# Performance work log

Hardware: AMD Instinct MI355X
Metric: run time of the kernel (lower is better)

## Reference

```python
import jax, jax.numpy as jnp
import numpy as np

D = 4544
H = 71
DKV = 64  # D // H
NKV = 1   # multi-query: one shared KV head
ROPE_BASE = 10000.0


def setup_inputs() -> dict:
    key = jax.random.key(0)
    k1, k2, k3 = jax.random.split(key, 3)
    N, L = 2, 1024
    hidden_states = jax.random.normal(k1, (N, L, D), dtype=jnp.float32)
    W_qkv = jax.random.normal(k2, (D + 2 * NKV * DKV, D), dtype=jnp.float32) * (D ** -0.5)
    W_dense = jax.random.normal(k3, (D, D), dtype=jnp.float32) * (D ** -0.5)
    return {"hidden_states": hidden_states, "W_qkv": W_qkv, "W_dense": W_dense}


def _rope_cos_sin(L, dtype):
    inv_freq = 1.0 / (ROPE_BASE ** (jnp.arange(0, DKV, 2, dtype=jnp.float32) / DKV))  # [Dkv/2]
    t = jnp.arange(L, dtype=jnp.float32)
    freqs = jnp.outer(t, inv_freq)                 # [L, Dkv/2]
    emb = jnp.concatenate((freqs, freqs), axis=1)  # [L, Dkv]
    cos = jnp.cos(emb)[None, None, :, :].astype(dtype)  # [1,1,L,Dkv]
    sin = jnp.sin(emb)[None, None, :, :].astype(dtype)
    return cos, sin


def _rotate_half(x):
    half = x.shape[-1] // 2
    return jnp.concatenate((-x[..., half:], x[..., :half]), axis=-1)


def reference(hidden_states, W_qkv, W_dense):
    N, L, _ = hidden_states.shape
    # Fused QKV projection (no bias): [N, L, D + 2*Dkv]
    fused = jnp.einsum('nld,ed->nle', hidden_states, W_qkv)
    fused = fused.reshape(N, L, H + 2 * NKV, DKV)
    query = jnp.transpose(fused[:, :, : H, :], (0, 2, 1, 3))            # [N, H, L, Dkv]
    key_h = jnp.transpose(fused[:, :, H : H + NKV, :], (0, 2, 1, 3))    # [N, 1, L, Dkv]
    value = jnp.transpose(fused[:, :, H + NKV :, :], (0, 2, 1, 3))      # [N, 1, L, Dkv]

    # RoPE (prefill path: positions 0..L-1)
    cos, sin = _rope_cos_sin(L, query.dtype)
    query = query * cos + _rotate_half(query) * sin
    key_h = key_h * cos + _rotate_half(key_h) * sin

    # Causal SDPA with multi-query KV broadcast (scale = 1/sqrt(Dkv))
    k = key_h[:, 0]    # [N, L, Dkv]
    v = value[:, 0]    # [N, L, Dkv]
    scale = 1.0 / jnp.sqrt(jnp.asarray(DKV, dtype=query.dtype))
    scores = jnp.einsum('nhqd,nkd->nhqk', query, k) * scale  # [N, H, L, L]
    causal = jnp.tril(jnp.ones((L, L), dtype=bool))
    scores = jnp.where(causal[None, None], scores, jnp.finfo(scores.dtype).min)
    weights = jax.nn.softmax(scores, axis=-1)
    attn = jnp.einsum('nhqk,nkd->nhqd', weights, v)           # [N, H, L, Dkv]

    attn = jnp.transpose(attn, (0, 2, 1, 3)).reshape(N, L, H * DKV)  # [N, L, D]
    out = jnp.einsum('nld,ed->nle', attn, W_dense)
    return out
```

## Files before the change

### kernel.cpp

```cpp
#include <hip/hip_runtime.h>

#define D_MODEL 4544
#define E_QKV   4672
#define E_STR   4736
#define E_PAD2  4864
#define D_PAD   4608
#define NH      71
#define SEQ     1024
#define NB      2
#define M_ROWS  2048

typedef __bf16 bf16_t;
typedef bf16_t bf16x8 __attribute__((ext_vector_type(8)));
typedef float f32x4 __attribute__((ext_vector_type(4)));
typedef float f32x16 __attribute__((ext_vector_type(16)));
typedef unsigned u32x4 __attribute__((ext_vector_type(4)));

typedef __attribute__((address_space(1))) const void* gas_ptr;
typedef __attribute__((address_space(3))) void* las_ptr;

static __device__ __forceinline__ unsigned short f2bf(float f) {
  union { float f; unsigned u; } v; v.f = f;
  unsigned r = (v.u + 0x7fffu + ((v.u >> 16) & 1u)) >> 16;
  return (unsigned short)r;
}

static __device__ __forceinline__ unsigned cvtpk_bf16(float lo, float hi) {
  unsigned r;
  asm("v_cvt_pk_bf16_f32 %0, %1, %2" : "=v"(r) : "v"(lo), "v"(hi));
  return r;
}

static __device__ __forceinline__ float fast_exp2(float x) {
  float r;
  asm("v_exp_f32 %0, %1" : "=v"(r) : "v"(x));
  return r;
}

__global__ void convert_pad(const float* __restrict__ src, unsigned short* __restrict__ dst,
                            int rows_src, int rows_pad, int cols) {
  int idx = blockIdx.x * 256 + threadIdx.x;
  int cols4 = cols >> 2;
  int total = rows_pad * cols4;
  if (idx >= total) return;
  int row = idx / cols4;
  int c4 = (idx - row * cols4) << 2;
  ushort4 o;
  if (row < rows_src) {
    const float4 v = *(const float4*)(src + (size_t)row * cols + c4);
    o.x = f2bf(v.x); o.y = f2bf(v.y); o.z = f2bf(v.z); o.w = f2bf(v.w);
  } else {
    o.x = 0; o.y = 0; o.z = 0; o.w = 0;
  }
  *(ushort4*)(dst + (size_t)row * cols + c4) = o;
}

#define REGION(b_, op_, kh_) (((((b_)*2+(op_))*2)+(kh_)) << 13)

#define STAGE(b_, op_, kh_, kt_) do {                                          \
  const unsigned short* _src = (op_) ? B : A;                                  \
  const size_t _rb = (op_) ? bCol : bRow;                                      \
  _Pragma("unroll")                                                            \
  for (int _ld = 0; _ld < 2; ++_ld) {                                          \
    int _ch = _ld * 512 + tid;                                                 \
    const unsigned short* _ga = _src + (_rb + (_ch >> 2)) * K                  \
                                + (kt_) * 64 + (kh_) * 32 + ((_ch & 3) << 3);  \
    __builtin_amdgcn_global_load_lds((gas_ptr)_ga,                             \
        (las_ptr)(lds + REGION(b_, op_, kh_) + ((_ld * 512 + wave * 64) << 3)),\
        16, 0, 0);                                                             \
  }                                                                            \
} while (0)

#define LDA4(b_, kh_, mh_) do {                                                \
  const unsigned short* _ab = lds + REGION(b_, 0, kh_);                        \
  _Pragma("unroll")                                                            \
  for (int _mm = 0; _mm < 4; ++_mm)                                            \
    a[_mm] = *(const bf16x8*)&_ab[(wm * 128 + (mh_) * 64 + _mm * 16 + c) * 32 + g * 8]; \
} while (0)

#define LDB4(b_, kh_) do {                                                     \
  const unsigned short* _bp = lds + REGION(b_, 1, kh_);                        \
  _Pragma("unroll")                                                            \
  for (int _n = 0; _n < 4; ++_n)                                               \
    bv[_n] = *(const bf16x8*)&_bp[(wn * 64 + _n * 16 + c) * 32 + g * 8];       \
} while (0)

#define MFMA16(mh_) do {                                                       \
  _Pragma("unroll")                                                            \
  for (int _mm = 0; _mm < 4; ++_mm)                                            \
    _Pragma("unroll")                                                          \
    for (int _n = 0; _n < 4; ++_n)                                             \
      acc[(mh_) * 4 + _mm][_n] = __builtin_amdgcn_mfma_f32_16x16x32_bf16(      \
          a[_mm], bv[_n], acc[(mh_) * 4 + _mm][_n], 0, 0, 0);                  \
} while (0)

__global__ __launch_bounds__(512, 2) void gemm256(
    const unsigned short* __restrict__ A,
    const unsigned short* __restrict__ B,
    float* __restrict__ C,
    int K, int Ntiles, int ldc, int Nact) {
  __shared__ __align__(16) unsigned short lds[65536];
  const int tid = threadIdx.x;
  const int wave = tid >> 6, lane = tid & 63;
  const int g = lane >> 4, c = lane & 15;
  const int wm = wave >> 2, wn = wave & 3;
  const int nwg = gridDim.x;
  const int swz = (blockIdx.x & 7) * (nwg >> 3) + (blockIdx.x >> 3);
  const int bm = swz / Ntiles, bn = swz - bm * Ntiles;
  const size_t bRow = (size_t)bm * 256, bCol = (size_t)bn * 256;
  const int NT = K >> 6;

  f32x4 acc[8][4] = {};

  STAGE(0, 0, 0, 0); STAGE(0, 1, 0, 0); STAGE(0, 0, 1, 0); STAGE(0, 1, 1, 0);
  STAGE(1, 1, 0, 1); STAGE(1, 0, 0, 1); STAGE(1, 1, 1, 1);
  asm volatile("s_waitcnt vmcnt(6)" ::: "memory");
  __builtin_amdgcn_s_barrier();

  for (int t = 0; t < NT; ++t) {
    const int b = t & 1;
    const int tn1 = (t + 1 < NT) ? t + 1 : 0;
    const int tn2 = (t + 2 < NT) ? t + 2 : 0;
    bf16x8 a[4], bv[4];
    LDA4(b, 0, 0); LDB4(b, 0);
    STAGE(b ^ 1, 0, 1, tn1);
    __builtin_amdgcn_s_barrier();
    asm volatile("s_waitcnt lgkmcnt(0)" ::: "memory");
    __builtin_amdgcn_s_setprio(1);
    MFMA16(0);
    __builtin_amdgcn_s_setprio(0);
    __builtin_amdgcn_s_barrier();
    LDA4(b, 0, 1);
    STAGE(b, 1, 0, tn2);
    __builtin_amdgcn_s_barrier();
    asm volatile("s_waitcnt lgkmcnt(0)" ::: "memory");
    __builtin_amdgcn_s_setprio(1);
    MFMA16(1);
    __builtin_amdgcn_s_setprio(0);
    __builtin_amdgcn_s_barrier();
    LDA4(b, 1, 0); LDB4(b, 1);
    STAGE(b, 0, 0, tn2);
    __builtin_amdgcn_s_barrier();
    asm volatile("s_waitcnt lgkmcnt(0)" ::: "memory");
    __builtin_amdgcn_s_setprio(1);
    MFMA16(0);
    __builtin_amdgcn_s_setprio(0);
    __builtin_amdgcn_s_barrier();
    LDA4(b, 1, 1);
    STAGE(b, 1, 1, tn2);
    __builtin_amdgcn_s_barrier();
    asm volatile("s_waitcnt lgkmcnt(0)" ::: "memory");
    __builtin_amdgcn_s_setprio(1);
    MFMA16(1);
    __builtin_amdgcn_s_setprio(0);
    asm volatile("s_waitcnt vmcnt(6)" ::: "memory");
    __builtin_amdgcn_s_barrier();
  }
  asm volatile("s_waitcnt vmcnt(0)" ::: "memory");

#pragma unroll
  for (int mm = 0; mm < 8; ++mm) {
#pragma unroll
    for (int n = 0; n < 4; ++n) {
      int col = (int)bCol + wn * 64 + n * 16 + c;
      if (col < Nact) {
#pragma unroll
        for (int r = 0; r < 4; ++r) {
          size_t row = bRow + wm * 128 + mm * 16 + g * 4 + r;
          C[row * ldc + col] = acc[mm][n][r];
        }
      }
    }
  }
}

__global__ void rope_extract(const float* __restrict__ fused,
                             unsigned short* __restrict__ Qb,
                             unsigned short* __restrict__ Kb,
                             unsigned short* __restrict__ VTb) {
  int idx = blockIdx.x * 256 + threadIdx.x;
  const int total = NB * SEQ * 73 * 64;
  if (idx >= total) return;
  int d = idx & 63;
  int t = idx >> 6;
  int h = t % 73;  t /= 73;
  int l = t & (SEQ - 1);
  int n = t >> 10;
  const float* frow = fused + ((size_t)(n * SEQ + l)) * E_STR + h * 64;
  float x = frow[d];
  if (h == 72) {
    VTb[((size_t)(n * 64 + d)) * SEQ + l] = f2bf(x);
    return;
  }
  int dh = d & 31;
  float inv = __expf(-(float)dh * (9.210340371976184f / 32.0f));
  float ang = (float)l * inv;
  float sn, cs;
  __sincosf(ang, &sn, &cs);
  float xr = frow[(d < 32) ? d + 32 : d - 32];
  float rh = (d < 32) ? -xr : xr;
  float out = x * cs + rh * sn;
  if (h == 71) {
    Kb[((size_t)(n * SEQ + l)) * 64 + d] = f2bf(out);
  } else {
    Qb[(((size_t)(n * NH + h)) * SEQ + l) * 64 + d] = f2bf(out * 0.1803368801111204f);
  }
}

__global__ __launch_bounds__(128) void attn_kernel(
    const unsigned short* __restrict__ Qb,
    const unsigned short* __restrict__ Kb,
    const unsigned short* __restrict__ VTb,
    unsigned short* __restrict__ attnb) {
  const int h = blockIdx.y, n = blockIdx.z;
  const int wave = threadIdx.x >> 6, lane = threadIdx.x & 63;
  const int c = lane & 31, hi = lane >> 5;
  const int gw = blockIdx.x * 2 + wave;

  const unsigned short* kbase = Kb + (size_t)n * SEQ * 64;
  const unsigned short* vtbase = VTb + (size_t)n * 64 * SEQ;

  for (int pass = 0; pass < 2; ++pass) {
    const int tile = pass ? gw : (31 - gw);
    const int qrow0 = tile * 32;
    const int q = qrow0 + c;
    const unsigned short* qbase = Qb + (((size_t)(n * NH + h)) * SEQ + qrow0) * 64;

    bf16x8 qf[4];
#pragma unroll
    for (int cc = 0; cc < 4; ++cc)
      qf[cc] = *(const bf16x8*)&qbase[c * 64 + cc * 16 + hi * 8];

    f32x16 o0 = {}, o1 = {};
    float m_run = -1e30f, l_run = 0.f;

    for (int kt = 0; kt < qrow0 + 32; kt += 64) {
      f32x16 s0 = {}, s1 = {};
#pragma unroll
      for (int cc = 0; cc < 4; ++cc) {
        bf16x8 k0 = *(const bf16x8*)&kbase[(size_t)(kt + c) * 64 + cc * 16 + hi * 8];
        bf16x8 k1 = *(const bf16x8*)&kbase[(size_t)(kt + 32 + c) * 64 + cc * 16 + hi * 8];
        s0 = __builtin_amdgcn_mfma_f32_32x32x16_bf16(k0, qf[cc], s0, 0, 0, 0);
        s1 = __builtin_amdgcn_mfma_f32_32x32x16_bf16(k1, qf[cc], s1, 0, 0, 0);
      }
      if (kt + 63 > qrow0) {
#pragma unroll
        for (int r = 0; r < 16; ++r) {
          const int key0 = kt + (r & 3) + 8 * (r >> 2) + 4 * hi;
          s0[r] = (key0 > q) ? -1e30f : s0[r];
          s1[r] = (key0 + 32 > q) ? -1e30f : s1[r];
        }
      }
      float tt[16];
#pragma unroll
      for (int r = 0; r < 16; ++r) tt[r] = fmaxf(s0[r], s1[r]);
#pragma unroll
      for (int st = 8; st > 0; st >>= 1)
#pragma unroll
        for (int r = 0; r < 8; ++r) if (r < st) tt[r] = fmaxf(tt[r], tt[r + st]);
      float mx = fmaxf(tt[0], __shfl_xor(tt[0], 32));
      const float mnew = fmaxf(m_run, mx);
      const float aa = fast_exp2(m_run - mnew);
#pragma unroll
      for (int r = 0; r < 16; ++r) {
        s0[r] = fast_exp2(s0[r] - mnew);
        s1[r] = fast_exp2(s1[r] - mnew);
      }
      float ps = 0.f;
#pragma unroll
      for (int r = 0; r < 16; ++r) ps += s0[r] + s1[r];
      ps += __shfl_xor(ps, 32);
      l_run = l_run * aa + ps;
      m_run = mnew;
#pragma unroll
      for (int r = 0; r < 16; ++r) { o0[r] *= aa; o1[r] *= aa; }

#pragma unroll
      for (int half = 0; half < 2; ++half) {
#pragma unroll
        for (int ccl = 0; ccl < 2; ++ccl) {
          const int cg = half * 2 + ccl;
          unsigned a0, a1, b0, b1;
          if (half == 0) {
            a0 = cvtpk_bf16(s0[8 * ccl + 0], s0[8 * ccl + 1]);
            a1 = cvtpk_bf16(s0[8 * ccl + 2], s0[8 * ccl + 3]);
            b0 = cvtpk_bf16(s0[8 * ccl + 4], s0[8 * ccl + 5]);
            b1 = cvtpk_bf16(s0[8 * ccl + 6], s0[8 * ccl + 7]);
          } else {
            a0 = cvtpk_bf16(s1[8 * ccl + 0], s1[8 * ccl + 1]);
            a1 = cvtpk_bf16(s1[8 * ccl + 2], s1[8 * ccl + 3]);
            b0 = cvtpk_bf16(s1[8 * ccl + 4], s1[8 * ccl + 5]);
            b1 = cvtpk_bf16(s1[8 * ccl + 6], s1[8 * ccl + 7]);
          }
          unsigned xa0 = __shfl_xor(a0, 32), xa1 = __shfl_xor(a1, 32);
          unsigned xb0 = __shfl_xor(b0, 32), xb1 = __shfl_xor(b1, 32);
          u32x4 fw;
          fw[0] = hi ? xb0 : a0;
          fw[1] = hi ? xb1 : a1;
          fw[2] = hi ? b0 : xa0;
          fw[3] = hi ? b1 : xa1;
          union { u32x4 u; bf16x8 b; } pf; pf.u = fw;
          bf16x8 v0 = *(const bf16x8*)&vtbase[(size_t)c * SEQ + kt + cg * 16 + hi * 8];
          bf16x8 v1 = *(const bf16x8*)&vtbase[(size_t)(32 + c) * SEQ + kt + cg * 16 + hi * 8];
          o0 = __builtin_amdgcn_mfma_f32_32x32x16_bf16(v0, pf.b, o0, 0, 0, 0);
          o1 = __builtin_amdgcn_mfma_f32_32x32x16_bf16(v1, pf.b, o1, 0, 0, 0);
        }
      }
    }

    const float inv = 1.0f / l_run;
    const size_t rowoff = (size_t)(n * SEQ + q) * D_MODEL + h * 64;
#pragma unroll
    for (int rr = 0; rr < 4; ++rr) {
      ushort4 w0, w1;
      w0.x = f2bf(o0[4 * rr + 0] * inv); w0.y = f2bf(o0[4 * rr + 1] * inv);
      w0.z = f2bf(o0[4 * rr + 2] * inv); w0.w = f2bf(o0[4 * rr + 3] * inv);
      w1.x = f2bf(o1[4 * rr + 0] * inv); w1.y = f2bf(o1[4 * rr + 1] * inv);
      w1.z = f2bf(o1[4 * rr + 2] * inv); w1.w = f2bf(o1[4 * rr + 3] * inv);
      *(ushort4*)&attnb[rowoff + 8 * rr + 4 * hi] = w0;
      *(ushort4*)&attnb[rowoff + 32 + 8 * rr + 4 * hi] = w1;
    }
  }
}

extern "C" void kernel_launch(void* const* d_in, const int* in_sizes, int n_in,
                              void* d_out, int out_size, void* d_ws, size_t ws_size,
                              hipStream_t stream) {
  const float* hs = (const float*)d_in[0];
  const float* wqkv = (const float*)d_in[1];
  const float* wdense = (const float*)d_in[2];
  float* out = (float*)d_out;
  char* ws = (char*)d_ws;

  unsigned short* hsb   = (unsigned short*)(ws + 0);
  unsigned short* wqkvb = (unsigned short*)(ws + 18612224);
  unsigned short* wdb   = (unsigned short*)(ws + 62820352);
  float*          fused = (float*)(ws + 104701952);
  unsigned short* qb    = (unsigned short*)(ws + 143499264);
  unsigned short* kb    = (unsigned short*)(ws + 162111488);
  unsigned short* vtb   = (unsigned short*)(ws + 162373632);
  unsigned short* attnb = (unsigned short*)(ws + 162635776);

  {
    int total = M_ROWS * (D_MODEL / 4);
    convert_pad<<<(total + 255) / 256, 256, 0, stream>>>(hs, hsb, M_ROWS, M_ROWS, D_MODEL);
  }
  {
    int total = E_PAD2 * (D_MODEL / 4);
    convert_pad<<<(total + 255) / 256, 256, 0, stream>>>(wqkv, wqkvb, E_QKV, E_PAD2, D_MODEL);
  }
  {
    int total = D_PAD * (D_MODEL / 4);
    convert_pad<<<(total + 255) / 256, 256, 0, stream>>>(wdense, wdb, D_MODEL, D_PAD, D_MODEL);
  }
  gemm256<<<dim3(8 * 19), 512, 0, stream>>>(hsb, wqkvb, fused, D_MODEL, 19, E_STR, E_STR);
  {
    int total = NB * SEQ * 73 * 64;
    rope_extract<<<(total + 255) / 256, 256, 0, stream>>>(fused, qb, kb, vtb);
  }
  attn_kernel<<<dim3(8, NH, NB), 128, 0, stream>>>(qb, kb, vtb, attnb);
  gemm256<<<dim3(8 * 18), 512, 0, stream>>>(attnb, wdb, out, D_MODEL, 18, D_MODEL, D_MODEL);
}
```

Baseline: 432.6 us.

## Split-K both GEMMs three ways and relayout LDS staging to MFMA fragment order

Both projection GEMMs are split into three K-chunks so the grids grow from 152 and 144 workgroups to three times that, which fills more compute units. The partial sums are written to separate workspace buffers. For the QKV projection they are summed inside rope_extract, and for the dense projection a new reduce3 kernel sums them. The LDS staging layout is also changed so each 16x32 fragment is stored contiguously and read as lane*8, which should cut address arithmetic and bank conflicts. In exchange this adds extra fp32 partial-output traffic and a reduction pass, and it depends on the workspace being large enough.

```diff
diff --git a/kernel.cpp b/kernel.cpp
--- a/kernel.cpp
+++ b/kernel.cpp
@@ -62,12 +62,11 @@
   const size_t _rb = (op_) ? bCol : bRow;                                      \
   _Pragma("unroll")                                                            \
   for (int _ld = 0; _ld < 2; ++_ld) {                                          \
-    int _ch = _ld * 512 + tid;                                                 \
-    const unsigned short* _ga = _src + (_rb + (_ch >> 2)) * K                  \
-                                + (kt_) * 64 + (kh_) * 32 + ((_ch & 3) << 3);  \
+    const int _fb = _ld * 8 + wave;                                            \
+    const unsigned short* _ga = _src + (_rb + _fb * 16 + c) * K                \
+                                + (kt_) * 64 + (kh_) * 32 + g * 8;             \
     __builtin_amdgcn_global_load_lds((gas_ptr)_ga,                             \
-        (las_ptr)(lds + REGION(b_, op_, kh_) + ((_ld * 512 + wave * 64) << 3)),\
-        16, 0, 0);                                                             \
+        (las_ptr)(lds + REGION(b_, op_, kh_) + (_fb << 9)), 16, 0, 0);         \
   }                                                                            \
 } while (0)
 
@@ -75,14 +74,14 @@
   const unsigned short* _ab = lds + REGION(b_, 0, kh_);                        \
   _Pragma("unroll")                                                            \
   for (int _mm = 0; _mm < 4; ++_mm)                                            \
-    a[_mm] = *(const bf16x8*)&_ab[(wm * 128 + (mh_) * 64 + _mm * 16 + c) * 32 + g * 8]; \
+    a[_mm] = *(const bf16x8*)&_ab[((wm * 8 + (mh_) * 4 + _mm) << 9) + lane * 8]; \
 } while (0)
 
 #define LDB4(b_, kh_) do {                                                     \
   const unsigned short* _bp = lds + REGION(b_, 1, kh_);                        \
   _Pragma("unroll")                                                            \
   for (int _n = 0; _n < 4; ++_n)                                               \
-    bv[_n] = *(const bf16x8*)&_bp[(wn * 64 + _n * 16 + c) * 32 + g * 8];       \
+    bv[_n] = *(const bf16x8*)&_bp[((wn * 4 + _n) << 9) + lane * 8];            \
 } while (0)
 
 #define MFMA16(mh_) do {                                                       \
@@ -97,8 +96,8 @@
 __global__ __launch_bounds__(512, 2) void gemm256(
     const unsigned short* __restrict__ A,
     const unsigned short* __restrict__ B,
-    float* __restrict__ C,
-    int K, int Ntiles, int ldc, int Nact) {
+    float* __restrict__ C0, float* __restrict__ C1, float* __restrict__ C2,
+    int K, int Ntiles, int ldc, int Nact, int chunk) {
   __shared__ __align__(16) unsigned short lds[65536];
   const int tid = threadIdx.x;
   const int wave = tid >> 6, lane = tid & 63;
@@ -106,21 +105,27 @@
   const int wm = wave >> 2, wn = wave & 3;
   const int nwg = gridDim.x;
   const int swz = (blockIdx.x & 7) * (nwg >> 3) + (blockIdx.x >> 3);
-  const int bm = swz / Ntiles, bn = swz - bm * Ntiles;
+  const int tilesTot = 8 * Ntiles;
+  const int kc = swz / tilesTot;
+  const int tile = swz - kc * tilesTot;
+  const int bm = tile / Ntiles, bn = tile - bm * Ntiles;
   const size_t bRow = (size_t)bm * 256, bCol = (size_t)bn * 256;
-  const int NT = K >> 6;
+  const int NTtot = K >> 6;
+  const int kb = kc * chunk;
+  const int nt = (NTtot - kb < chunk) ? (NTtot - kb) : chunk;
+  float* __restrict__ C = (kc == 0) ? C0 : ((kc == 1) ? C1 : C2);
 
   f32x4 acc[8][4] = {};
 
-  STAGE(0, 0, 0, 0); STAGE(0, 1, 0, 0); STAGE(0, 0, 1, 0); STAGE(0, 1, 1, 0);
-  STAGE(1, 1, 0, 1); STAGE(1, 0, 0, 1); STAGE(1, 1, 1, 1);
+  STAGE(0, 0, 0, kb); STAGE(0, 1, 0, kb); STAGE(0, 0, 1, kb); STAGE(0, 1, 1, kb);
+  STAGE(1, 1, 0, kb + 1); STAGE(1, 0, 0, kb + 1); STAGE(1, 1, 1, kb + 1);
   asm volatile("s_waitcnt vmcnt(6)" ::: "memory");
   __builtin_amdgcn_s_barrier();
 
-  for (int t = 0; t < NT; ++t) {
+  for (int t = 0; t < nt; ++t) {
     const int b = t & 1;
-    const int tn1 = (t + 1 < NT) ? t + 1 : 0;
-    const int tn2 = (t + 2 < NT) ? t + 2 : 0;
+    const int tn1 = kb + ((t + 1 < nt) ? t + 1 : 0);
+    const int tn2 = kb + ((t + 2 < nt) ? t + 2 : 0);
     bf16x8 a[4], bv[4];
     LDA4(b, 0, 0); LDB4(b, 0);
     STAGE(b ^ 1, 0, 1, tn1);
@@ -174,7 +179,21 @@
   }
 }
 
-__global__ void rope_extract(const float* __restrict__ fused,
+__global__ void reduce3(const float* __restrict__ p0, const float* __restrict__ p1,
+                        const float* __restrict__ p2, float* __restrict__ out, int total4) {
+  int idx = blockIdx.x * 256 + threadIdx.x;
+  if (idx >= total4) return;
+  float4 a = *(const float4*)(p0 + (size_t)idx * 4);
+  float4 b = *(const float4*)(p1 + (size_t)idx * 4);
+  float4 cc = *(const float4*)(p2 + (size_t)idx * 4);
+  float4 o;
+  o.x = a.x + b.x + cc.x; o.y = a.y + b.y + cc.y;
+  o.z = a.z + b.z + cc.z; o.w = a.w + b.w + cc.w;
+  *(float4*)(out + (size_t)idx * 4) = o;
+}
+
+__global__ void rope_extract(const float* __restrict__ p0, const float* __restrict__ p1,
+                             const float* __restrict__ p2, int np,
                              unsigned short* __restrict__ Qb,
                              unsigned short* __restrict__ Kb,
                              unsigned short* __restrict__ VTb) {
@@ -186,8 +205,9 @@
   int h = t % 73;  t /= 73;
   int l = t & (SEQ - 1);
   int n = t >> 10;
-  const float* frow = fused + ((size_t)(n * SEQ + l)) * E_STR + h * 64;
-  float x = frow[d];
+  const size_t base = ((size_t)(n * SEQ + l)) * E_STR + h * 64;
+  float x = p0[base + d];
+  if (np == 3) x += p1[base + d] + p2[base + d];
   if (h == 72) {
     VTb[((size_t)(n * 64 + d)) * SEQ + l] = f2bf(x);
     return;
@@ -197,8 +217,9 @@
   float ang = (float)l * inv;
   float sn, cs;
   __sincosf(ang, &sn, &cs);
-  float xr = frow[(d < 32) ? d + 32 : d - 32];
-  float rh = (d < 32) ? -xr : xr;
+  float xr0 = p0[base + ((d < 32) ? d + 32 : d - 32)];
+  if (np == 3) xr0 += p1[base + ((d < 32) ? d + 32 : d - 32)] + p2[base + ((d < 32) ? d + 32 : d - 32)];
+  float rh = (d < 32) ? -xr0 : xr0;
   float out = x * cs + rh * sn;
   if (h == 71) {
     Kb[((size_t)(n * SEQ + l)) * 64 + d] = f2bf(out);
@@ -340,6 +361,9 @@
   unsigned short* kb    = (unsigned short*)(ws + 162111488);
   unsigned short* vtb   = (unsigned short*)(ws + 162373632);
   unsigned short* attnb = (unsigned short*)(ws + 162635776);
+  float* fusedE1 = (float*)(ws + 181248000);
+  float* fusedE2 = (float*)(ws + 220045312);
+  const int splitOK = (ws_size >= (size_t)258842624) ? 1 : 0;
 
   {
     int total = M_ROWS * (D_MODEL / 4);
@@ -353,11 +377,30 @@
     int total = D_PAD * (D_MODEL / 4);
     convert_pad<<<(total + 255) / 256, 256, 0, stream>>>(wdense, wdb, D_MODEL, D_PAD, D_MODEL);
   }
-  gemm256<<<dim3(8 * 19), 512, 0, stream>>>(hsb, wqkvb, fused, D_MODEL, 19, E_STR, E_STR);
+
+  if (splitOK) {
+    gemm256<<<dim3(8 * 19 * 3), 512, 0, stream>>>(hsb, wqkvb, fused, fusedE1, fusedE2,
+                                                  D_MODEL, 19, E_STR, E_STR, 24);
+  } else {
+    gemm256<<<dim3(8 * 19), 512, 0, stream>>>(hsb, wqkvb, fused, fused, fused,
+                                              D_MODEL, 19, E_STR, E_STR, 71);
+  }
   {
     int total = NB * SEQ * 73 * 64;
-    rope_extract<<<(total + 255) / 256, 256, 0, stream>>>(fused, qb, kb, vtb);
+    rope_extract<<<(total + 255) / 256, 256, 0, stream>>>(fused, fusedE1, fusedE2,
+                                                          splitOK ? 3 : 1, qb, kb, vtb);
   }
   attn_kernel<<<dim3(8, NH, NB), 128, 0, stream>>>(qb, kb, vtb, attnb);
-  gemm256<<<dim3(8 * 18), 512, 0, stream>>>(attnb, wdb, out, D_MODEL, 18, D_MODEL, D_MODEL);
-}
+  if (splitOK) {
+    float* p0 = (float*)(ws + 0);
+    float* p1 = fused;
+    float* p2 = fusedE1;
+    gemm256<<<dim3(8 * 18 * 3), 512, 0, stream>>>(attnb, wdb, p0, p1, p2,
+                                                  D_MODEL, 18, D_MODEL, D_MODEL, 24);
+    int total4 = (M_ROWS * D_MODEL) / 4;
+    reduce3<<<(total4 + 255) / 256, 256, 0, stream>>>(p0, p1, p2, out, total4);
+  } else {
+    gemm256<<<dim3(8 * 18), 512, 0, stream>>>(attnb, wdb, out, out, out,
+                                              D_MODEL, 18, D_MODEL, D_MODEL, 71);
+  }
+}
```

Result: no change. 433.2 us (+0.2%).

## Restructure GEMM main loop: fragment-ordered LDS layout and single barrier pair per tile

Applied to the files above, without the earlier changes.

Changes the global-to-LDS staging so each 16-row fragment is stored contiguously in the order MFMA lanes read it, letting each lane's LDS read be a linear lane*8 offset with fewer bank conflicts. The K-tile loop is rebuilt to load all A/B fragments into registers up front, interleave them with MFMAs, then issue all four next-next stages after a single barrier, replacing the previous eight barriers per tile. This raises register pressure (six fragment arrays live at once) and drops the final vmcnt(0) drain, relying on the trailing wraparound loads being harmless.

```diff
diff --git a/kernel.cpp b/kernel.cpp
--- a/kernel.cpp
+++ b/kernel.cpp
@@ -62,36 +62,35 @@
   const size_t _rb = (op_) ? bCol : bRow;                                      \
   _Pragma("unroll")                                                            \
   for (int _ld = 0; _ld < 2; ++_ld) {                                          \
-    int _ch = _ld * 512 + tid;                                                 \
-    const unsigned short* _ga = _src + (_rb + (_ch >> 2)) * K                  \
-                                + (kt_) * 64 + (kh_) * 32 + ((_ch & 3) << 3);  \
+    const int _fb = _ld * 8 + wave;                                            \
+    const unsigned short* _ga = _src + (_rb + _fb * 16 + c) * K                \
+                                + (kt_) * 64 + (kh_) * 32 + g * 8;             \
     __builtin_amdgcn_global_load_lds((gas_ptr)_ga,                             \
-        (las_ptr)(lds + REGION(b_, op_, kh_) + ((_ld * 512 + wave * 64) << 3)),\
-        16, 0, 0);                                                             \
+        (las_ptr)(lds + REGION(b_, op_, kh_) + (_fb << 9)), 16, 0, 0);         \
   }                                                                            \
 } while (0)
 
-#define LDA4(b_, kh_, mh_) do {                                                \
+#define LDA4G(dst_, b_, kh_, mh_) do {                                         \
   const unsigned short* _ab = lds + REGION(b_, 0, kh_);                        \
   _Pragma("unroll")                                                            \
   for (int _mm = 0; _mm < 4; ++_mm)                                            \
-    a[_mm] = *(const bf16x8*)&_ab[(wm * 128 + (mh_) * 64 + _mm * 16 + c) * 32 + g * 8]; \
+    dst_[_mm] = *(const bf16x8*)&_ab[((wm * 8 + (mh_) * 4 + _mm) << 9) + lane * 8]; \
 } while (0)
 
-#define LDB4(b_, kh_) do {                                                     \
+#define LDB4G(dst_, b_, kh_) do {                                              \
   const unsigned short* _bp = lds + REGION(b_, 1, kh_);                        \
   _Pragma("unroll")                                                            \
   for (int _n = 0; _n < 4; ++_n)                                               \
-    bv[_n] = *(const bf16x8*)&_bp[(wn * 64 + _n * 16 + c) * 32 + g * 8];       \
+    dst_[_n] = *(const bf16x8*)&_bp[((wn * 4 + _n) << 9) + lane * 8];          \
 } while (0)
 
-#define MFMA16(mh_) do {                                                       \
+#define MFMA16G(af_, bf_, mh_) do {                                            \
   _Pragma("unroll")                                                            \
   for (int _mm = 0; _mm < 4; ++_mm)                                            \
     _Pragma("unroll")                                                          \
     for (int _n = 0; _n < 4; ++_n)                                             \
       acc[(mh_) * 4 + _mm][_n] = __builtin_amdgcn_mfma_f32_16x16x32_bf16(      \
-          a[_mm], bv[_n], acc[(mh_) * 4 + _mm][_n], 0, 0, 0);                  \
+          af_[_mm], bf_[_n], acc[(mh_) * 4 + _mm][_n], 0, 0, 0);               \
 } while (0)
 
 __global__ __launch_bounds__(512, 2) void gemm256(
@@ -113,50 +112,36 @@
   f32x4 acc[8][4] = {};
 
   STAGE(0, 0, 0, 0); STAGE(0, 1, 0, 0); STAGE(0, 0, 1, 0); STAGE(0, 1, 1, 0);
-  STAGE(1, 1, 0, 1); STAGE(1, 0, 0, 1); STAGE(1, 1, 1, 1);
-  asm volatile("s_waitcnt vmcnt(6)" ::: "memory");
+  STAGE(1, 0, 0, 1); STAGE(1, 1, 0, 1); STAGE(1, 0, 1, 1); STAGE(1, 1, 1, 1);
+  asm volatile("s_waitcnt vmcnt(8)" ::: "memory");
   __builtin_amdgcn_s_barrier();
 
   for (int t = 0; t < NT; ++t) {
     const int b = t & 1;
-    const int tn1 = (t + 1 < NT) ? t + 1 : 0;
     const int tn2 = (t + 2 < NT) ? t + 2 : 0;
-    bf16x8 a[4], bv[4];
-    LDA4(b, 0, 0); LDB4(b, 0);
-    STAGE(b ^ 1, 0, 1, tn1);
+    bf16x8 fa0[4], fa1[4], fa2[4], fa3[4], fb0[4], fb1[4];
+    LDA4G(fa0, b, 0, 0); LDB4G(fb0, b, 0);
+    LDA4G(fa1, b, 0, 1);
+    __builtin_amdgcn_s_setprio(1);
+    MFMA16G(fa0, fb0, 0);
+    __builtin_amdgcn_s_setprio(0);
+    LDA4G(fa2, b, 1, 0); LDB4G(fb1, b, 1);
+    __builtin_amdgcn_s_setprio(1);
+    MFMA16G(fa1, fb0, 1);
+    __builtin_amdgcn_s_setprio(0);
+    LDA4G(fa3, b, 1, 1);
+    __builtin_amdgcn_s_setprio(1);
+    MFMA16G(fa2, fb1, 0);
+    MFMA16G(fa3, fb1, 1);
+    __builtin_amdgcn_s_setprio(0);
+    asm volatile("" ::: "memory");
     __builtin_amdgcn_s_barrier();
-    asm volatile("s_waitcnt lgkmcnt(0)" ::: "memory");
-    __builtin_amdgcn_s_setprio(1);
-    MFMA16(0);
-    __builtin_amdgcn_s_setprio(0);
+    asm volatile("" ::: "memory");
+    STAGE(b, 0, 0, tn2); STAGE(b, 1, 0, tn2);
+    STAGE(b, 0, 1, tn2); STAGE(b, 1, 1, tn2);
+    asm volatile("s_waitcnt vmcnt(8)" ::: "memory");
     __builtin_amdgcn_s_barrier();
-    LDA4(b, 0, 1);
-    STAGE(b, 1, 0, tn2);
-    __builtin_amdgcn_s_barrier();
-    asm volatile("s_waitcnt lgkmcnt(0)" ::: "memory");
-    __builtin_amdgcn_s_setprio(1);
-    MFMA16(1);
-    __builtin_amdgcn_s_setprio(0);
-    __builtin_amdgcn_s_barrier();
-    LDA4(b, 1, 0); LDB4(b, 1);
-    STAGE(b, 0, 0, tn2);
-    __builtin_amdgcn_s_barrier();
-    asm volatile("s_waitcnt lgkmcnt(0)" ::: "memory");
-    __builtin_amdgcn_s_setprio(1);
-    MFMA16(0);
-    __builtin_amdgcn_s_setprio(0);
-    __builtin_amdgcn_s_barrier();
-    LDA4(b, 1, 1);
-    STAGE(b, 1, 1, tn2);
-    __builtin_amdgcn_s_barrier();
-    asm volatile("s_waitcnt lgkmcnt(0)" ::: "memory");
-    __builtin_amdgcn_s_setprio(1);
-    MFMA16(1);
-    __builtin_amdgcn_s_setprio(0);
-    asm volatile("s_waitcnt vmcnt(6)" ::: "memory");
-    __builtin_amdgcn_s_barrier();
-  }
-  asm volatile("s_waitcnt vmcnt(0)" ::: "memory");
+  }
 
 #pragma unroll
   for (int mm = 0; mm < 8; ++mm) {
```

Measured after the change: 552.1 us. 27.6% more time.

## Split-K GEMMs three ways with atomic accumulation and precompute per-thread load pointers

Applied to the files above, without the earlier changes.

Both projection GEMMs now split the K dimension into three chunks of 24 tiles, launching three times as many workgroups. Partial sums are combined with float atomicAdd into outputs that are zeroed first by memsets. The aim is to fill the 256 CUs, which 152/144 workgroups leave underused. STAGE and the LDS read addressing were also simplified by precomputing per-thread global pointers and storing each 16-row block contiguously. The trade-off is extra atomic traffic, two memsets, and results that are no longer deterministic.

```diff
diff --git a/kernel.cpp b/kernel.cpp
--- a/kernel.cpp
+++ b/kernel.cpp
@@ -58,31 +58,27 @@
 #define REGION(b_, op_, kh_) (((((b_)*2+(op_))*2)+(kh_)) << 13)
 
 #define STAGE(b_, op_, kh_, kt_) do {                                          \
-  const unsigned short* _src = (op_) ? B : A;                                  \
-  const size_t _rb = (op_) ? bCol : bRow;                                      \
-  _Pragma("unroll")                                                            \
-  for (int _ld = 0; _ld < 2; ++_ld) {                                          \
-    int _ch = _ld * 512 + tid;                                                 \
-    const unsigned short* _ga = _src + (_rb + (_ch >> 2)) * K                  \
-                                + (kt_) * 64 + (kh_) * 32 + ((_ch & 3) << 3);  \
-    __builtin_amdgcn_global_load_lds((gas_ptr)_ga,                             \
-        (las_ptr)(lds + REGION(b_, op_, kh_) + ((_ld * 512 + wave * 64) << 3)),\
-        16, 0, 0);                                                             \
-  }                                                                            \
+  const unsigned short* _p0 = (op_) ? pB0 : pA0;                               \
+  const unsigned short* _p1 = (op_) ? pB1 : pA1;                               \
+  const int _koff = ((kt_) << 6) + ((kh_) << 5);                               \
+  __builtin_amdgcn_global_load_lds((gas_ptr)(_p0 + _koff),                     \
+      (las_ptr)(lds + REGION(b_, op_, kh_) + (wave << 9)), 16, 0, 0);          \
+  __builtin_amdgcn_global_load_lds((gas_ptr)(_p1 + _koff),                     \
+      (las_ptr)(lds + REGION(b_, op_, kh_) + ((8 + wave) << 9)), 16, 0, 0);    \
 } while (0)
 
 #define LDA4(b_, kh_, mh_) do {                                                \
   const unsigned short* _ab = lds + REGION(b_, 0, kh_);                        \
   _Pragma("unroll")                                                            \
   for (int _mm = 0; _mm < 4; ++_mm)                                            \
-    a[_mm] = *(const bf16x8*)&_ab[(wm * 128 + (mh_) * 64 + _mm * 16 + c) * 32 + g * 8]; \
+    a[_mm] = *(const bf16x8*)&_ab[((wm * 8 + (mh_) * 4 + _mm) << 9) + lane * 8]; \
 } while (0)
 
 #define LDB4(b_, kh_) do {                                                     \
   const unsigned short* _bp = lds + REGION(b_, 1, kh_);                        \
   _Pragma("unroll")                                                            \
   for (int _n = 0; _n < 4; ++_n)                                               \
-    bv[_n] = *(const bf16x8*)&_bp[(wn * 64 + _n * 16 + c) * 32 + g * 8];       \
+    bv[_n] = *(const bf16x8*)&_bp[((wn * 4 + _n) << 9) + lane * 8];            \
 } while (0)
 
 #define MFMA16(mh_) do {                                                       \
@@ -98,7 +94,7 @@
     const unsigned short* __restrict__ A,
     const unsigned short* __restrict__ B,
     float* __restrict__ C,
-    int K, int Ntiles, int ldc, int Nact) {
+    int K, int Ntiles, int ldc, int Nact, int chunk) {
   __shared__ __align__(16) unsigned short lds[65536];
   const int tid = threadIdx.x;
   const int wave = tid >> 6, lane = tid & 63;
@@ -106,21 +102,31 @@
   const int wm = wave >> 2, wn = wave & 3;
   const int nwg = gridDim.x;
   const int swz = (blockIdx.x & 7) * (nwg >> 3) + (blockIdx.x >> 3);
-  const int bm = swz / Ntiles, bn = swz - bm * Ntiles;
+  const int tilesTot = 8 * Ntiles;
+  const int kc = swz / tilesTot;
+  const int tile = swz - kc * tilesTot;
+  const int bm = tile / Ntiles, bn = tile - bm * Ntiles;
   const size_t bRow = (size_t)bm * 256, bCol = (size_t)bn * 256;
-  const int NT = K >> 6;
+  const int NTtot = K >> 6;
+  const int kb = kc * chunk;
+  const int nt = (NTtot - kb < chunk) ? (NTtot - kb) : chunk;
+
+  const unsigned short* pA0 = A + (bRow + (size_t)(wave * 16 + c)) * K + g * 8;
+  const unsigned short* pA1 = A + (bRow + (size_t)((8 + wave) * 16 + c)) * K + g * 8;
+  const unsigned short* pB0 = B + (bCol + (size_t)(wave * 16 + c)) * K + g * 8;
+  const unsigned short* pB1 = B + (bCol + (size_t)((8 + wave) * 16 + c)) * K + g * 8;
 
   f32x4 acc[8][4] = {};
 
-  STAGE(0, 0, 0, 0); STAGE(0, 1, 0, 0); STAGE(0, 0, 1, 0); STAGE(0, 1, 1, 0);
-  STAGE(1, 1, 0, 1); STAGE(1, 0, 0, 1); STAGE(1, 1, 1, 1);
+  STAGE(0, 0, 0, kb); STAGE(0, 1, 0, kb); STAGE(0, 0, 1, kb); STAGE(0, 1, 1, kb);
+  STAGE(1, 1, 0, kb + 1); STAGE(1, 0, 0, kb + 1); STAGE(1, 1, 1, kb + 1);
   asm volatile("s_waitcnt vmcnt(6)" ::: "memory");
   __builtin_amdgcn_s_barrier();
 
-  for (int t = 0; t < NT; ++t) {
+  for (int t = 0; t < nt; ++t) {
     const int b = t & 1;
-    const int tn1 = (t + 1 < NT) ? t + 1 : 0;
-    const int tn2 = (t + 2 < NT) ? t + 2 : 0;
+    const int tn1 = kb + ((t + 1 < nt) ? t + 1 : 0);
+    const int tn2 = kb + ((t + 2 < nt) ? t + 2 : 0);
     bf16x8 a[4], bv[4];
     LDA4(b, 0, 0); LDB4(b, 0);
     STAGE(b ^ 1, 0, 1, tn1);
@@ -167,7 +173,7 @@
 #pragma unroll
         for (int r = 0; r < 4; ++r) {
           size_t row = bRow + wm * 128 + mm * 16 + g * 4 + r;
-          C[row * ldc + col] = acc[mm][n][r];
+          atomicAdd(&C[row * ldc + col], acc[mm][n][r]);
         }
       }
     }
@@ -341,6 +347,9 @@
   unsigned short* vtb   = (unsigned short*)(ws + 162373632);
   unsigned short* attnb = (unsigned short*)(ws + 162635776);
 
+  hipMemsetAsync(fused, 0, (size_t)M_ROWS * E_STR * 4, stream);
+  hipMemsetAsync(out, 0, (size_t)out_size * 4, stream);
+
   {
     int total = M_ROWS * (D_MODEL / 4);
     convert_pad<<<(total + 255) / 256, 256, 0, stream>>>(hs, hsb, M_ROWS, M_ROWS, D_MODEL);
@@ -353,11 +362,14 @@
     int total = D_PAD * (D_MODEL / 4);
     convert_pad<<<(total + 255) / 256, 256, 0, stream>>>(wdense, wdb, D_MODEL, D_PAD, D_MODEL);
   }
-  gemm256<<<dim3(8 * 19), 512, 0, stream>>>(hsb, wqkvb, fused, D_MODEL, 19, E_STR, E_STR);
+
+  gemm256<<<dim3(8 * 19 * 3), 512, 0, stream>>>(hsb, wqkvb, fused,
+                                                D_MODEL, 19, E_STR, E_STR, 24);
   {
     int total = NB * SEQ * 73 * 64;
     rope_extract<<<(total + 255) / 256, 256, 0, stream>>>(fused, qb, kb, vtb);
   }
   attn_kernel<<<dim3(8, NH, NB), 128, 0, stream>>>(qb, kb, vtb, attnb);
-  gemm256<<<dim3(8 * 18), 512, 0, stream>>>(attnb, wdb, out, D_MODEL, 18, D_MODEL, D_MODEL);
-}
+  gemm256<<<dim3(8 * 18 * 3), 512, 0, stream>>>(attnb, wdb, out,
+                                                D_MODEL, 18, D_MODEL, D_MODEL, 24);
+}
```

Result: slower. 532.3 us (+23.1%).
